# Performance work log

Hardware: AMD Instinct MI355X
Metric: run time of the kernel (lower is better)

## Reference

```python
import jax, jax.numpy as jnp
import numpy as np
from numpy.polynomial import Polynomial

H = 1.0    # knot spacing (init arg h)
T0 = 0.0   # left endpoint (init arg t0)
N_SAMPLES = 131072
N_KNOTS = 2048
Q = 3      # spline order -> q+1 local basis polynomials


def build_basis(h: float, q: int):
    # Faithful port of the torch module's recursive B-spline basis construction.
    o = Polynomial([0.0]); e = Polynomial([1.0]); x = Polynomial([0.0, 1.0])
    B = np.empty((q + 1, q + 1), dtype=object)
    for i in range(q + 1):
        for j in range(q + 1):
            B[i, j] = o
    B[0, 0] = e
    for p in range(1, q + 1):
        for i in range(p + 1):
            B[p, i] += B[p - 1, i] * x
            if i:
                B[p, i] += B[p - 1, i - 1](x - h) * (h * (p + 1) - x)
            B[p, i] /= h * p
    return [B[-1, i] for i in range(q + 1)]


def basis_coeff_matrix(h: float, q: int) -> np.ndarray:
    # Matches buffer_from_polynomes('B', ...): rows are polynomes[::-1],
    # coefficients in ascending power order (Polynomial.coef convention).
    polys = build_basis(h, q)
    M = np.zeros((q + 1, q + 1), dtype=np.float32)
    for j, poly in enumerate(polys[::-1]):
        c = np.asarray(poly.coef, dtype=np.float64)
        M[j, :len(c)] = c.astype(np.float32)
    return M


def setup_inputs() -> dict:
    key = jax.random.key(0)
    # samples inside the spline support so most knot indices are in-range
    xs = jax.random.uniform(key, (N_SAMPLES,), dtype=jnp.float32,
                            minval=0.0, maxval=(N_KNOTS - Q) * H)
    B = jnp.asarray(basis_coeff_matrix(H, Q))  # [q+1, q+1]
    return {"xs": xs, "B": B, "n": N_KNOTS, "q": Q}


def reference(xs, B, n, q):
    # xs: [N] float32, B: [q+1, q+1] ascending-power coeffs, n/q: python ints
    x = xs - T0
    first_i = jnp.floor(x / H).astype(jnp.int32)          # [N] knot bin index
    offs = jnp.arange(q + 1)
    cols = first_i[:, None] + offs[None, :]               # [N, q+1]
    # local coordinate for each of the q+1 overlapping basis polynomials
    x_loc = (x - first_i.astype(xs.dtype) * H)[:, None] + H * (q - offs)[None, :].astype(xs.dtype)
    # power series 0..q, then dot with coefficient rows: values[n,k] = sum_p x_loc^p * B[k,p]
    powers = x_loc[:, :, None] ** jnp.arange(q + 1)       # [N, q+1, q+1]
    values = jnp.einsum('nkp,kp->nk', powers, B)          # [N, q+1]
    valid = (cols >= 0) & (cols < n)
    cols_c = jnp.clip(cols, 0, n - 1)
    rows = jnp.arange(xs.shape[0])[:, None]
    out = jnp.zeros((xs.shape[0], n), dtype=xs.dtype)
    out = out.at[rows, cols_c].add(jnp.where(valid, values, jnp.zeros_like(values)))
    return out
```

## Files before the change

### kernel.cpp

```cpp
#include <hip/hip_runtime.h>


__global__ __launch_bounds__(256) void bspline_row_kernel(
    const float* __restrict__ xs,
    const float* __restrict__ B,
    float* __restrict__ out,
    int n_knots) {
    const int row = blockIdx.x;
    const float x = xs[row];
    const float fif = floorf(x);
    const int fi = (int)fif;
    const float frac = x - fif;

    float v0, v1, v2, v3;
    {
        float t;
        t = frac + 3.0f; v0 = ((B[0*4+3]*t + B[0*4+2])*t + B[0*4+1])*t + B[0*4+0];
        t = frac + 2.0f; v1 = ((B[1*4+3]*t + B[1*4+2])*t + B[1*4+1])*t + B[1*4+0];
        t = frac + 1.0f; v2 = ((B[2*4+3]*t + B[2*4+2])*t + B[2*4+1])*t + B[2*4+0];
        t = frac + 0.0f; v3 = ((B[3*4+3]*t + B[3*4+2])*t + B[3*4+1])*t + B[3*4+0];
    }

    float* outrow = out + (size_t)row * (size_t)n_knots;

    const int nvec = n_knots & ~3;
    for (int c = threadIdx.x * 4; c < nvec; c += blockDim.x * 4) {
        float4 w = make_float4(0.0f, 0.0f, 0.0f, 0.0f);
        if (c + 3 >= fi && c <= fi + 3) {
            float* wp = (float*)&w;
            #pragma unroll
            for (int j = 0; j < 4; ++j) {
                const int k = (c + j) - fi;
                float val = 0.0f;
                if (k == 0) val = v0;
                else if (k == 1) val = v1;
                else if (k == 2) val = v2;
                else if (k == 3) val = v3;
                wp[j] = val;
            }
        }
        *(float4*)(outrow + c) = w;
    }
    for (int c = nvec + (int)threadIdx.x; c < n_knots; c += (int)blockDim.x) {
        const int k = c - fi;
        float val = 0.0f;
        if (k == 0) val = v0;
        else if (k == 1) val = v1;
        else if (k == 2) val = v2;
        else if (k == 3) val = v3;
        outrow[c] = val;
    }
}

extern "C" void kernel_launch(void* const* d_in, const int* in_sizes, int n_in,
                              void* d_out, int out_size, void* d_ws, size_t ws_size,
                              hipStream_t stream) {
    const float* xs = (const float*)d_in[0];
    const float* B  = (const float*)d_in[1];
    float* out = (float*)d_out;

    const int n_samples = in_sizes[0];
    const int n_knots   = out_size / n_samples;

    bspline_row_kernel<<<n_samples, 256, 0, stream>>>(xs, B, out, n_knots);
}
```

Before: 1.013 ms.

## Zero-fill row chunks with nontemporal stores, then scatter four spline values

Each block now handles 32 rows instead of one. It zero-fills the contiguous chunk with nontemporal vector stores, synchronises, and then each thread writes its row's four basis values with scalar stores. This takes the per-element window test out of the fill loop, cuts the block count, and keeps the 1 GB of zeros from polluting the cache. In exchange each nonzero element is written twice, and correctness relies on the zero stores being visible before the later scalar stores, which the barrier is meant to guarantee.

```diff
diff --git a/kernel.cpp b/kernel.cpp
--- a/kernel.cpp
+++ b/kernel.cpp
@@ -1,54 +1,54 @@
 #include <hip/hip_runtime.h>
 
 
-__global__ __launch_bounds__(256) void bspline_row_kernel(
+constexpr int BLOCK = 256;
+constexpr int ROWS_PER_BLOCK = 32;
+
+typedef float floatx4 __attribute__((ext_vector_type(4)));
+
+__global__ __launch_bounds__(BLOCK) void bspline_fill_kernel(
     const float* __restrict__ xs,
     const float* __restrict__ B,
     float* __restrict__ out,
+    int n_samples,
     int n_knots) {
-    const int row = blockIdx.x;
-    const float x = xs[row];
-    const float fif = floorf(x);
-    const int fi = (int)fif;
-    const float frac = x - fif;
+    const int tid = threadIdx.x;
+    const int base_row = blockIdx.x * ROWS_PER_BLOCK;
+    const int rows = min(ROWS_PER_BLOCK, n_samples - base_row);
 
-    float v0, v1, v2, v3;
-    {
-        float t;
-        t = frac + 3.0f; v0 = ((B[0*4+3]*t + B[0*4+2])*t + B[0*4+1])*t + B[0*4+0];
-        t = frac + 2.0f; v1 = ((B[1*4+3]*t + B[1*4+2])*t + B[1*4+1])*t + B[1*4+0];
-        t = frac + 1.0f; v2 = ((B[2*4+3]*t + B[2*4+2])*t + B[2*4+1])*t + B[2*4+0];
-        t = frac + 0.0f; v3 = ((B[3*4+3]*t + B[3*4+2])*t + B[3*4+1])*t + B[3*4+0];
+    float x = 0.0f;
+    if (tid < rows) x = xs[base_row + tid];
+
+    float* chunk = out + (size_t)base_row * (size_t)n_knots;
+    const size_t nfloats = (size_t)rows * (size_t)n_knots;
+
+    const size_t nvec = nfloats & ~(size_t)3;
+    const floatx4 z = {0.0f, 0.0f, 0.0f, 0.0f};
+    for (size_t f = (size_t)tid * 4; f < nvec; f += (size_t)BLOCK * 4) {
+        __builtin_nontemporal_store(z, (floatx4*)(chunk + f));
+    }
+    for (size_t f = nvec + (size_t)tid; f < nfloats; f += (size_t)BLOCK) {
+        chunk[f] = 0.0f;
     }
 
-    float* outrow = out + (size_t)row * (size_t)n_knots;
+    __syncthreads();
 
-    const int nvec = n_knots & ~3;
-    for (int c = threadIdx.x * 4; c < nvec; c += blockDim.x * 4) {
-        float4 w = make_float4(0.0f, 0.0f, 0.0f, 0.0f);
-        if (c + 3 >= fi && c <= fi + 3) {
-            float* wp = (float*)&w;
-            #pragma unroll
-            for (int j = 0; j < 4; ++j) {
-                const int k = (c + j) - fi;
-                float val = 0.0f;
-                if (k == 0) val = v0;
-                else if (k == 1) val = v1;
-                else if (k == 2) val = v2;
-                else if (k == 3) val = v3;
-                wp[j] = val;
-            }
+    if (tid < rows) {
+        const float fif = floorf(x);
+        const int fi = (int)fif;
+        const float frac = x - fif;
+        float t, v0, v1, v2, v3;
+        t = frac + 3.0f; v0 = ((B[ 3]*t + B[ 2])*t + B[ 1])*t + B[ 0];
+        t = frac + 2.0f; v1 = ((B[ 7]*t + B[ 6])*t + B[ 5])*t + B[ 4];
+        t = frac + 1.0f; v2 = ((B[11]*t + B[10])*t + B[ 9])*t + B[ 8];
+        t = frac;        v3 = ((B[15]*t + B[14])*t + B[13])*t + B[12];
+        const float vals[4] = {v0, v1, v2, v3};
+        float* rowp = chunk + (size_t)tid * (size_t)n_knots;
+        #pragma unroll
+        for (int k = 0; k < 4; ++k) {
+            const int c = fi + k;
+            if (c >= 0 && c < n_knots) rowp[c] = vals[k];
         }
-        *(float4*)(outrow + c) = w;
-    }
-    for (int c = nvec + (int)threadIdx.x; c < n_knots; c += (int)blockDim.x) {
-        const int k = c - fi;
-        float val = 0.0f;
-        if (k == 0) val = v0;
-        else if (k == 1) val = v1;
-        else if (k == 2) val = v2;
-        else if (k == 3) val = v3;
-        outrow[c] = val;
     }
 }
 
@@ -62,5 +62,6 @@
     const int n_samples = in_sizes[0];
     const int n_knots   = out_size / n_samples;
 
-    bspline_row_kernel<<<n_samples, 256, 0, stream>>>(xs, B, out, n_knots);
+    const int grid = (n_samples + ROWS_PER_BLOCK - 1) / ROWS_PER_BLOCK;
+    bspline_fill_kernel<<<grid, BLOCK, 0, stream>>>(xs, B, out, n_samples, n_knots);
 }
```

Measured after the change: 1.068 ms. 1.05x slower.
